# Kernel optimization log

Measured on AMD Instinct MI355X. Metric: run time of the kernel, lower is better.

Reference implementation:

```python
import jax, jax.numpy as jnp
import numpy as np

B, S, H = 64, 2048, 512
NEG = -1e9

def setup_inputs() -> dict:
    key = jax.random.key(0)
    k1, k2, k3, k4, k5 = jax.random.split(key, 5)
    encoder_outputs = jax.random.normal(k1, (B, S, H), dtype=jnp.float32)
    mask = jax.random.randint(k2, (B, S), 0, 2).astype(bool)
    W = jax.random.normal(k3, (H, H), dtype=jnp.float32) / np.sqrt(H)
    b = jnp.zeros((H,), dtype=jnp.float32)
    v = jax.random.normal(k4, (H,), dtype=jnp.float32)  # context_vector
    return {"encoder_outputs": encoder_outputs, "mask": mask, "W": W, "b": b, "v": v}

def reference(encoder_outputs, mask, W, b, v):
    # u = tanh(x @ W^T + b): [B,S,H]
    u = jnp.tanh(jnp.einsum('bsh,oh->bso', encoder_outputs, W) + b)
    scores = jnp.einsum('bsh,h->bs', u, v)                 # [B,S]
    scores = jnp.where(mask, scores, NEG)
    attn_weights = jax.nn.softmax(scores, axis=1)          # [B,S]
    weighted_output = jnp.einsum('bsh,bs->bh', encoder_outputs, attn_weights)
    return weighted_output, attn_weights
```

## Files before the change

kernel.cpp:

```cpp
#include <hip/hip_runtime.h>
#include <hip/hip_fp16.h>
#include <stdint.h>

#define NEG_ (-1e9f)

typedef _Float16 f16x8 __attribute__((ext_vector_type(8)));
typedef float    f32x4 __attribute__((ext_vector_type(4)));

__device__ __forceinline__ float fast_tanh(float x) {
  float e = __expf(2.0f * x);
  return (e - 1.0f) * __builtin_amdgcn_rcpf(e + 1.0f);
}

__global__ __launch_bounds__(256) void k0_cvt_w(const float* __restrict__ W,
                                                __half* __restrict__ Wws) {
  int g = blockIdx.x * 256 + threadIdx.x;
  int lane = g & 63;
  int seg  = g >> 6;
  int io = seg & 3, ks = (seg >> 2) & 15, w = seg >> 6;
  int o = w * 64 + io * 16 + (lane & 15);
  int k = ks * 32 + (lane >> 4) * 8;
  const float2* src = (const float2*)(W + (size_t)o * 512 + k);
  __half2 h[4];
#pragma unroll
  for (int j = 0; j < 4; ++j) { float2 f = src[j]; h[j] = __floats2half2_rn(f.x, f.y); }
  uint4 u;
  u.x = *(uint32_t*)&h[0]; u.y = *(uint32_t*)&h[1];
  u.z = *(uint32_t*)&h[2]; u.w = *(uint32_t*)&h[3];
  *(uint4*)(Wws + (size_t)seg * 512 + (size_t)lane * 8) = u;
}

__global__ __launch_bounds__(512, 4) void k1_scores(
    const float* __restrict__ enc, const int* __restrict__ msk,
    const float* __restrict__ bias, const float* __restrict__ ctx,
    const __half* __restrict__ Wws, float* __restrict__ scores,
    float* __restrict__ psum, float* __restrict__ mpart,
    float* __restrict__ lpart) {
  __shared__ __align__(16) __half Xl[64 * 512];
  __shared__ float sred[512];
  __shared__ float pbuf[64];

  const int t = threadIdx.x;
  const int w = t >> 6;
  const int lane = t & 63;
  const int quad = lane >> 4;
  const int l15 = lane & 15;
  const size_t mtile = blockIdx.x;

  f16x8 abuf[3][4];
  auto aload = [&](int slot, int ks) {
    const f16x8* sp = (const f16x8*)(Wws +
        ((size_t)(w * 64 + ks * 4) * 512) + (size_t)lane * 8);
#pragma unroll
    for (int io = 0; io < 4; ++io) abuf[slot][io] = sp[io * 64];
  };

  {
    const float4* Xg = (const float4*)(enc + mtile * (size_t)(64 * 512));
    float4 xr[16];
#pragma unroll
    for (int j = 0; j < 8; ++j) {
      int g = j * 512 + t;
      int s = g >> 6, c = g & 63;
      xr[2 * j]     = Xg[s * 128 + 2 * c];
      xr[2 * j + 1] = Xg[s * 128 + 2 * c + 1];
    }
    aload(0, 0);
    aload(1, 1);
#pragma unroll
    for (int j = 0; j < 8; ++j) {
      int g = j * 512 + t;
      int s = g >> 6, c = g & 63;
      float4 x0 = xr[2 * j];
      float4 x1 = xr[2 * j + 1];
      __half2 h0 = __floats2half2_rn(x0.x, x0.y);
      __half2 h1 = __floats2half2_rn(x0.z, x0.w);
      __half2 h2 = __floats2half2_rn(x1.x, x1.y);
      __half2 h3 = __floats2half2_rn(x1.z, x1.w);
      uint4 u;
      u.x = *(uint32_t*)&h0; u.y = *(uint32_t*)&h1;
      u.z = *(uint32_t*)&h2; u.w = *(uint32_t*)&h3;
      int pc = c ^ (s & 7);
      *(uint4*)&Xl[s * 512 + pc * 8] = u;
    }
  }
  __syncthreads();

  f32x4 acc[4][4];
#pragma unroll
  for (int io = 0; io < 4; ++io)
#pragma unroll
    for (int is = 0; is < 4; ++is) acc[io][is] = (f32x4){0.f, 0.f, 0.f, 0.f};

#pragma unroll
  for (int ks = 0; ks < 16; ++ks) {
    if (ks + 2 < 16) aload((ks + 2) % 3, ks + 2);
    const f16x8* acur = abuf[ks % 3];
#pragma unroll
    for (int is = 0; is < 4; ++is) {
      int s = is * 16 + l15;
      const f16x8 bf = *(const f16x8*)&Xl[s * 512 + (((ks * 4 + quad) ^ (s & 7)) << 3)];
#pragma unroll
      for (int io = 0; io < 4; ++io)
        acc[io][is] = __builtin_amdgcn_mfma_f32_16x16x32_f16(acur[io], bf, acc[io][is], 0, 0, 0);
    }
  }

  float ps[4] = {0.f, 0.f, 0.f, 0.f};
#pragma unroll
  for (int io = 0; io < 4; ++io) {
    int ob = w * 64 + io * 16 + quad * 4;
    float4 b4 = *(const float4*)(bias + ob);
    float4 v4 = *(const float4*)(ctx + ob);
#pragma unroll
    for (int is = 0; is < 4; ++is) {
      const f32x4 a = acc[io][is];
      ps[is] += fast_tanh(a[0] + b4.x) * v4.x + fast_tanh(a[1] + b4.y) * v4.y +
                fast_tanh(a[2] + b4.z) * v4.z + fast_tanh(a[3] + b4.w) * v4.w;
    }
  }
#pragma unroll
  for (int is = 0; is < 4; ++is) {
    ps[is] += __shfl_xor(ps[is], 16, 64);
    ps[is] += __shfl_xor(ps[is], 32, 64);
  }

  __syncthreads();
  if (lane < 16) {
#pragma unroll
    for (int is = 0; is < 4; ++is) sred[w * 64 + is * 16 + lane] = ps[is];
  }
  __syncthreads();
  if (t < 64) {
    float sc = 0.f;
#pragma unroll
    for (int k = 0; k < 8; ++k) sc += sred[k * 64 + t];
    size_t row = mtile * 64 + t;
    float sm = msk[row] ? sc : NEG_;
    scores[row] = sm;
    float m = sm;
#pragma unroll
    for (int off = 32; off >= 1; off >>= 1) m = fmaxf(m, __shfl_xor(m, off, 64));
    float p = __expf(sm - m);
    float l = p;
#pragma unroll
    for (int off = 32; off >= 1; off >>= 1) l += __shfl_xor(l, off, 64);
    pbuf[t] = p;
    if (t == 0) { mpart[mtile] = m; lpart[mtile] = l; }
  }
  __syncthreads();

  float pacc[8] = {0.f, 0.f, 0.f, 0.f, 0.f, 0.f, 0.f, 0.f};
  const int c = lane;
#pragma unroll
  for (int si = 0; si < 8; ++si) {
    int s = (w << 3) + si;
    float pv = pbuf[s];
    f16x8 xv = *(const f16x8*)&Xl[s * 512 + ((c ^ (s & 7)) << 3)];
#pragma unroll
    for (int j = 0; j < 8; ++j) pacc[j] = fmaf(pv, (float)xv[j], pacc[j]);
  }
  __syncthreads();
  float* pred = (float*)&Xl[0];
  {
    float4 lo = {pacc[0], pacc[1], pacc[2], pacc[3]};
    float4 hi = {pacc[4], pacc[5], pacc[6], pacc[7]};
    *(float4*)&pred[w * 512 + c * 4] = lo;
    *(float4*)&pred[w * 512 + 256 + c * 4] = hi;
  }
  __syncthreads();
  if (t < 128) {
    int half = t & 1, c2 = t >> 1;
    float4 a = {0.f, 0.f, 0.f, 0.f};
#pragma unroll
    for (int w2 = 0; w2 < 8; ++w2) {
      float4 pv = *(const float4*)&pred[w2 * 512 + half * 256 + c2 * 4];
      a.x += pv.x; a.y += pv.y; a.z += pv.z; a.w += pv.w;
    }
    *(float4*)&psum[mtile * 512 + (size_t)t * 4] = a;
  }
}

__global__ __launch_bounds__(256) void k2_combine(
    float* __restrict__ attn, const float* __restrict__ psum,
    const float* __restrict__ mpart, const float* __restrict__ lpart,
    float* __restrict__ out0) {
  const int b = blockIdx.x, t = threadIdx.x;
  __shared__ float ml[32], ll[32];
  if (t < 32) { ml[t] = mpart[b * 32 + t]; ll[t] = lpart[b * 32 + t]; }
  __syncthreads();
  float M = -3.4e38f;
#pragma unroll
  for (int i = 0; i < 32; ++i) M = fmaxf(M, ml[i]);
  float wgt[32];
  float Z = 0.f;
#pragma unroll
  for (int i = 0; i < 32; ++i) {
    float e = __expf(ml[i] - M);
    wgt[i] = e;
    Z += e * ll[i];
  }
  float invZ = 1.0f / Z;
  float* row = attn + (size_t)b * 2048;
#pragma unroll
  for (int i = 0; i < 8; ++i) {
    int s = t + 256 * i;
    row[s] = __expf(row[s] - M) * invZ;
  }
  if (t < 128) {
    float4 a = {0.f, 0.f, 0.f, 0.f};
#pragma unroll
    for (int c2 = 0; c2 < 32; ++c2) {
      float wv = wgt[c2];
      float4 p = *(const float4*)&psum[((size_t)(b * 32 + c2)) * 512 + (size_t)t * 4];
      a.x = fmaf(wv, p.x, a.x);
      a.y = fmaf(wv, p.y, a.y);
      a.z = fmaf(wv, p.z, a.z);
      a.w = fmaf(wv, p.w, a.w);
    }
    float4 r = {a.x * invZ, a.y * invZ, a.z * invZ, a.w * invZ};
    *(float4*)&out0[(size_t)b * 512 + (size_t)t * 4] = r;
  }
}

extern "C" void kernel_launch(void* const* d_in, const int* in_sizes, int n_in,
                              void* d_out, int out_size, void* d_ws, size_t ws_size,
                              hipStream_t stream) {
  (void)in_sizes; (void)n_in; (void)out_size; (void)ws_size;
  const float* enc  = (const float*)d_in[0];
  const int*   msk  = (const int*)d_in[1];
  const float* W    = (const float*)d_in[2];
  const float* bias = (const float*)d_in[3];
  const float* ctx  = (const float*)d_in[4];
  float* out0 = (float*)d_out;
  float* attn = out0 + 64 * 512;

  __half* Wws  = (__half*)d_ws;
  float*  psum = (float*)((char*)d_ws + (512u << 10));
  float*  mprt = psum + (size_t)2048 * 512;
  float*  lprt = mprt + 2048;

  k0_cvt_w<<<128, 256, 0, stream>>>(W, Wws);
  k1_scores<<<2048, 512, 0, stream>>>(enc, msk, bias, ctx, Wws, attn,
                                      psum, mprt, lprt);
  k2_combine<<<64, 256, 0, stream>>>(attn, psum, mprt, lprt, out0);
}
```

Measured before the change: 444.4 us.

## Process four M-tiles per block and prefetch next tile's input during epilogue

Each k1 block now loops over four 64-row tiles instead of one, launching a quarter as many blocks. The global loads for the next tile are issued right after the MFMA loop, so they overlap the tanh, softmax and weighted-sum epilogue, and the data is converted and written to LDS at the end of the iteration. The goal is to hide HBM latency and cut per-block launch and setup cost. In exchange, 512 blocks may underfill the GPU's CUs, extra registers hold the prefetched data, and the launch-bounds occupancy hint is removed.

```diff
diff --git a/kernel.cpp b/kernel.cpp
--- a/kernel.cpp
+++ b/kernel.cpp
@@ -3,6 +3,7 @@
 #include <stdint.h>
 
 #define NEG_ (-1e9f)
+#define TILES 4
 
 typedef _Float16 f16x8 __attribute__((ext_vector_type(8)));
 typedef float    f32x4 __attribute__((ext_vector_type(4)));
@@ -10,6 +11,12 @@
 __device__ __forceinline__ float fast_tanh(float x) {
   float e = __expf(2.0f * x);
   return (e - 1.0f) * __builtin_amdgcn_rcpf(e + 1.0f);
+}
+
+__device__ __forceinline__ void bar_lds() {
+  asm volatile("s_waitcnt lgkmcnt(0)" ::: "memory");
+  __builtin_amdgcn_s_barrier();
+  __builtin_amdgcn_sched_barrier(0);
 }
 
 __global__ __launch_bounds__(256) void k0_cvt_w(const float* __restrict__ W,
@@ -30,7 +37,7 @@
   *(uint4*)(Wws + (size_t)seg * 512 + (size_t)lane * 8) = u;
 }
 
-__global__ __launch_bounds__(512, 4) void k1_scores(
+__global__ __launch_bounds__(512) void k1_scores(
     const float* __restrict__ enc, const int* __restrict__ msk,
     const float* __restrict__ bias, const float* __restrict__ ctx,
     const __half* __restrict__ Wws, float* __restrict__ scores,
@@ -45,7 +52,7 @@
   const int lane = t & 63;
   const int quad = lane >> 4;
   const int l15 = lane & 15;
-  const size_t mtile = blockIdx.x;
+  const size_t m0 = (size_t)blockIdx.x * TILES;
 
   f16x8 abuf[3][4];
   auto aload = [&](int slot, int ks) {
@@ -55,24 +62,21 @@
     for (int io = 0; io < 4; ++io) abuf[slot][io] = sp[io * 64];
   };
 
-  {
-    const float4* Xg = (const float4*)(enc + mtile * (size_t)(64 * 512));
-    float4 xr[16];
+  float4 xr[16];
+  uint4  xh[8];
+  auto xissue = [&](size_t mt) {
+    const float4* Xg = (const float4*)(enc + mt * (size_t)(64 * 512));
 #pragma unroll
     for (int j = 0; j < 8; ++j) {
-      int g = j * 512 + t;
-      int s = g >> 6, c = g & 63;
-      xr[2 * j]     = Xg[s * 128 + 2 * c];
-      xr[2 * j + 1] = Xg[s * 128 + 2 * c + 1];
-    }
-    aload(0, 0);
-    aload(1, 1);
+      int s = 8 * j + w;
+      xr[2 * j]     = Xg[s * 128 + 2 * lane];
+      xr[2 * j + 1] = Xg[s * 128 + 2 * lane + 1];
+    }
+  };
+  auto xconv = [&]() {
 #pragma unroll
     for (int j = 0; j < 8; ++j) {
-      int g = j * 512 + t;
-      int s = g >> 6, c = g & 63;
-      float4 x0 = xr[2 * j];
-      float4 x1 = xr[2 * j + 1];
+      float4 x0 = xr[2 * j], x1 = xr[2 * j + 1];
       __half2 h0 = __floats2half2_rn(x0.x, x0.y);
       __half2 h1 = __floats2half2_rn(x0.z, x0.w);
       __half2 h2 = __floats2half2_rn(x1.x, x1.y);
@@ -80,104 +84,133 @@
       uint4 u;
       u.x = *(uint32_t*)&h0; u.y = *(uint32_t*)&h1;
       u.z = *(uint32_t*)&h2; u.w = *(uint32_t*)&h3;
-      int pc = c ^ (s & 7);
-      *(uint4*)&Xl[s * 512 + pc * 8] = u;
-    }
-  }
-  __syncthreads();
-
-  f32x4 acc[4][4];
-#pragma unroll
-  for (int io = 0; io < 4; ++io)
-#pragma unroll
-    for (int is = 0; is < 4; ++is) acc[io][is] = (f32x4){0.f, 0.f, 0.f, 0.f};
-
-#pragma unroll
-  for (int ks = 0; ks < 16; ++ks) {
-    if (ks + 2 < 16) aload((ks + 2) % 3, ks + 2);
-    const f16x8* acur = abuf[ks % 3];
+      xh[j] = u;
+    }
+  };
+  auto xwrite = [&]() {
+#pragma unroll
+    for (int j = 0; j < 8; ++j) {
+      int s = 8 * j + w;
+      int pc = lane ^ (s & 7);
+      *(uint4*)&Xl[s * 512 + pc * 8] = xh[j];
+    }
+  };
+
+  xissue(m0);
+  xconv();
+  xwrite();
+  bar_lds();
+
+#pragma unroll 1
+  for (int i = 0; i < TILES; ++i) {
+    const size_t mtile = m0 + i;
+
+    aload(0, 0);
+    aload(1, 1);
+
+    f32x4 acc[4][4];
+#pragma unroll
+    for (int io = 0; io < 4; ++io)
+#pragma unroll
+      for (int is = 0; is < 4; ++is) acc[io][is] = (f32x4){0.f, 0.f, 0.f, 0.f};
+
+#pragma unroll
+    for (int ks = 0; ks < 16; ++ks) {
+      if (ks + 2 < 16) aload((ks + 2) % 3, ks + 2);
+      const f16x8* acur = abuf[ks % 3];
+#pragma unroll
+      for (int is = 0; is < 4; ++is) {
+        int s = is * 16 + l15;
+        const f16x8 bf = *(const f16x8*)&Xl[s * 512 + (((ks * 4 + quad) ^ (s & 7)) << 3)];
+#pragma unroll
+        for (int io = 0; io < 4; ++io)
+          acc[io][is] = __builtin_amdgcn_mfma_f32_16x16x32_f16(acur[io], bf, acc[io][is], 0, 0, 0);
+      }
+    }
+
+    __builtin_amdgcn_sched_barrier(0);
+    if (i + 1 < TILES) xissue(mtile + 1);
+
+    float ps[4] = {0.f, 0.f, 0.f, 0.f};
+#pragma unroll
+    for (int io = 0; io < 4; ++io) {
+      int ob = w * 64 + io * 16 + quad * 4;
+      float4 b4 = *(const float4*)(bias + ob);
+      float4 v4 = *(const float4*)(ctx + ob);
+#pragma unroll
+      for (int is = 0; is < 4; ++is) {
+        const f32x4 a = acc[io][is];
+        ps[is] += fast_tanh(a[0] + b4.x) * v4.x + fast_tanh(a[1] + b4.y) * v4.y +
+                  fast_tanh(a[2] + b4.z) * v4.z + fast_tanh(a[3] + b4.w) * v4.w;
+      }
+    }
 #pragma unroll
     for (int is = 0; is < 4; ++is) {
-      int s = is * 16 + l15;
-      const f16x8 bf = *(const f16x8*)&Xl[s * 512 + (((ks * 4 + quad) ^ (s & 7)) << 3)];
-#pragma unroll
-      for (int io = 0; io < 4; ++io)
-        acc[io][is] = __builtin_amdgcn_mfma_f32_16x16x32_f16(acur[io], bf, acc[io][is], 0, 0, 0);
-    }
-  }
-
-  float ps[4] = {0.f, 0.f, 0.f, 0.f};
-#pragma unroll
-  for (int io = 0; io < 4; ++io) {
-    int ob = w * 64 + io * 16 + quad * 4;
-    float4 b4 = *(const float4*)(bias + ob);
-    float4 v4 = *(const float4*)(ctx + ob);
-#pragma unroll
-    for (int is = 0; is < 4; ++is) {
-      const f32x4 a = acc[io][is];
-      ps[is] += fast_tanh(a[0] + b4.x) * v4.x + fast_tanh(a[1] + b4.y) * v4.y +
-                fast_tanh(a[2] + b4.z) * v4.z + fast_tanh(a[3] + b4.w) * v4.w;
-    }
-  }
-#pragma unroll
-  for (int is = 0; is < 4; ++is) {
-    ps[is] += __shfl_xor(ps[is], 16, 64);
-    ps[is] += __shfl_xor(ps[is], 32, 64);
-  }
-
-  __syncthreads();
-  if (lane < 16) {
-#pragma unroll
-    for (int is = 0; is < 4; ++is) sred[w * 64 + is * 16 + lane] = ps[is];
-  }
-  __syncthreads();
-  if (t < 64) {
-    float sc = 0.f;
-#pragma unroll
-    for (int k = 0; k < 8; ++k) sc += sred[k * 64 + t];
-    size_t row = mtile * 64 + t;
-    float sm = msk[row] ? sc : NEG_;
-    scores[row] = sm;
-    float m = sm;
-#pragma unroll
-    for (int off = 32; off >= 1; off >>= 1) m = fmaxf(m, __shfl_xor(m, off, 64));
-    float p = __expf(sm - m);
-    float l = p;
-#pragma unroll
-    for (int off = 32; off >= 1; off >>= 1) l += __shfl_xor(l, off, 64);
-    pbuf[t] = p;
-    if (t == 0) { mpart[mtile] = m; lpart[mtile] = l; }
-  }
-  __syncthreads();
-
-  float pacc[8] = {0.f, 0.f, 0.f, 0.f, 0.f, 0.f, 0.f, 0.f};
-  const int c = lane;
-#pragma unroll
-  for (int si = 0; si < 8; ++si) {
-    int s = (w << 3) + si;
-    float pv = pbuf[s];
-    f16x8 xv = *(const f16x8*)&Xl[s * 512 + ((c ^ (s & 7)) << 3)];
-#pragma unroll
-    for (int j = 0; j < 8; ++j) pacc[j] = fmaf(pv, (float)xv[j], pacc[j]);
-  }
-  __syncthreads();
-  float* pred = (float*)&Xl[0];
-  {
-    float4 lo = {pacc[0], pacc[1], pacc[2], pacc[3]};
-    float4 hi = {pacc[4], pacc[5], pacc[6], pacc[7]};
-    *(float4*)&pred[w * 512 + c * 4] = lo;
-    *(float4*)&pred[w * 512 + 256 + c * 4] = hi;
-  }
-  __syncthreads();
-  if (t < 128) {
-    int half = t & 1, c2 = t >> 1;
-    float4 a = {0.f, 0.f, 0.f, 0.f};
-#pragma unroll
-    for (int w2 = 0; w2 < 8; ++w2) {
-      float4 pv = *(const float4*)&pred[w2 * 512 + half * 256 + c2 * 4];
-      a.x += pv.x; a.y += pv.y; a.z += pv.z; a.w += pv.w;
-    }
-    *(float4*)&psum[mtile * 512 + (size_t)t * 4] = a;
+      ps[is] += __shfl_xor(ps[is], 16, 64);
+      ps[is] += __shfl_xor(ps[is], 32, 64);
+    }
+
+    bar_lds();
+    if (lane < 16) {
+#pragma unroll
+      for (int is = 0; is < 4; ++is) sred[w * 64 + is * 16 + lane] = ps[is];
+    }
+    bar_lds();
+    if (t < 64) {
+      float sc = 0.f;
+#pragma unroll
+      for (int k = 0; k < 8; ++k) sc += sred[k * 64 + t];
+      size_t row = mtile * 64 + t;
+      float sm = msk[row] ? sc : NEG_;
+      scores[row] = sm;
+      float m = sm;
+#pragma unroll
+      for (int off = 32; off >= 1; off >>= 1) m = fmaxf(m, __shfl_xor(m, off, 64));
+      float p = __expf(sm - m);
+      float l = p;
+#pragma unroll
+      for (int off = 32; off >= 1; off >>= 1) l += __shfl_xor(l, off, 64);
+      pbuf[t] = p;
+      if (t == 0) { mpart[mtile] = m; lpart[mtile] = l; }
+    }
+    bar_lds();
+
+    float pacc[8] = {0.f, 0.f, 0.f, 0.f, 0.f, 0.f, 0.f, 0.f};
+    const int c = lane;
+#pragma unroll
+    for (int si = 0; si < 8; ++si) {
+      int s = (w << 3) + si;
+      float pv = pbuf[s];
+      f16x8 xv = *(const f16x8*)&Xl[s * 512 + ((c ^ (s & 7)) << 3)];
+#pragma unroll
+      for (int j = 0; j < 8; ++j) pacc[j] = fmaf(pv, (float)xv[j], pacc[j]);
+    }
+    bar_lds();
+    float* pred = (float*)&Xl[0];
+    {
+      float4 lo = {pacc[0], pacc[1], pacc[2], pacc[3]};
+      float4 hi = {pacc[4], pacc[5], pacc[6], pacc[7]};
+      *(float4*)&pred[w * 512 + c * 4] = lo;
+      *(float4*)&pred[w * 512 + 256 + c * 4] = hi;
+    }
+    bar_lds();
+    if (t < 128) {
+      int half = t & 1, c2 = t >> 1;
+      float4 a = {0.f, 0.f, 0.f, 0.f};
+#pragma unroll
+      for (int w2 = 0; w2 < 8; ++w2) {
+        float4 pv = *(const float4*)&pred[w2 * 512 + half * 256 + c2 * 4];
+        a.x += pv.x; a.y += pv.y; a.z += pv.z; a.w += pv.w;
+      }
+      *(float4*)&psum[mtile * 512 + (size_t)t * 4] = a;
+    }
+    bar_lds();
+
+    if (i + 1 < TILES) {
+      xconv();
+      xwrite();
+    }
+    bar_lds();
   }
 }
 
@@ -241,7 +274,7 @@
   float*  lprt = mprt + 2048;
 
   k0_cvt_w<<<128, 256, 0, stream>>>(W, Wws);
-  k1_scores<<<2048, 512, 0, stream>>>(enc, msk, bias, ctx, Wws, attn,
-                                      psum, mprt, lprt);
+  k1_scores<<<2048 / TILES, 512, 0, stream>>>(enc, msk, bias, ctx, Wws, attn,
+                                              psum, mprt, lprt);
   k2_combine<<<64, 256, 0, stream>>>(attn, psum, mprt, lprt, out0);
 }
```

Result: slower. 623.5 us (+40.3%).
